# Optimization experiments

Measured on AMD Instinct MI355X. Metric: run time of the kernel, lower is better.

## Reference

```python
import jax, jax.numpy as jnp
import numpy as np

NUM_HEADS = 8
HEAD_DIM = 64


def setup_inputs() -> dict:
    key = jax.random.key(0)
    k1, k2, k3 = jax.random.split(key, 3)
    B, T, S, D = 2, 32, 1024, 512
    inner = NUM_HEADS * HEAD_DIM  # 512
    x = jax.random.normal(k1, (B, T, S, D), dtype=jnp.float32)
    W_qkv = jax.random.normal(k2, (D, 3 * inner), dtype=jnp.float32) * (D ** -0.5)
    W_out = jax.random.normal(k3, (inner, D), dtype=jnp.float32) * (inner ** -0.5)
    return {"x": x, "W_qkv": W_qkv, "W_out": W_out}


def reference(x, W_qkv, W_out):
    # x: (B, T, S, D); causal attention over T at each spatial position S.
    B, T, S, D = x.shape
    H, hd = NUM_HEADS, HEAD_DIM
    scale = hd ** -0.5
    qkv = jnp.einsum('btsd,de->btse', x, W_qkv)  # (B,T,S,3*H*hd)
    qkv = qkv.reshape(B, T, S, 3, H, hd)
    q, k, v = qkv[..., 0, :, :], qkv[..., 1, :, :], qkv[..., 2, :, :]  # (B,T,S,H,hd)
    # attention logits per (batch, spatial, head): (B,S,H,Tq,Tk)
    attn = jnp.einsum('bqshd,bkshd->bshqk', q, k) * scale
    causal_mask = jnp.triu(jnp.ones((T, T), dtype=bool), 1)  # True above diagonal
    attn = jnp.where(causal_mask, -jnp.inf, attn)
    attn = jax.nn.softmax(attn, axis=-1)
    out = jnp.einsum('bshqk,bkshd->bqshd', attn, v)  # (B,T,S,H,hd)
    out = out.reshape(B, T, S, H * hd)
    return jnp.einsum('btse,ed->btsd', out, W_out)  # (B,T,S,D)
```

## Files before the change

kernel.cpp:

```cpp
#include <hip/hip_runtime.h>
#include <cstdint>
#include <cstddef>

#define KDIM 512

typedef __attribute__((ext_vector_type(8))) __bf16 bf16x8;
typedef __attribute__((ext_vector_type(8))) unsigned short ushort8;
typedef __attribute__((ext_vector_type(4))) float f32x4;
typedef unsigned short u16;

__device__ __forceinline__ float bf2f(u16 u) {
  union { unsigned u32; float f; } x; x.u32 = ((unsigned)u) << 16; return x.f;
}
__device__ __forceinline__ u16 f2bf(float f) {
  union { float f; unsigned u; } x; x.f = f;
  unsigned u = x.u;
  unsigned r = (u + 0x7fffu + ((u >> 16) & 1u)) >> 16;
  return (u16)r;
}

__global__ __launch_bounds__(256) void cast_x_kernel(const float* __restrict__ in,
                                                     u16* __restrict__ out, int n4) {
  int i = blockIdx.x * 256 + threadIdx.x;
  if (i >= n4) return;
  float4 v = ((const float4*)in)[i];
  ushort4 o;
  o.x = f2bf(v.x); o.y = f2bf(v.y); o.z = f2bf(v.z); o.w = f2bf(v.w);
  ((ushort4*)out)[i] = o;
}

__global__ __launch_bounds__(256) void transpose_cast_kernel(const float* __restrict__ in,
                                                             u16* __restrict__ out,
                                                             int R, int C) {
  int o = blockIdx.x * 256 + threadIdx.x;
  if (o >= R * C) return;
  int r = o % R;
  int c = o / R;
  out[o] = f2bf(in[(size_t)r * C + c]);
}

__device__ __forceinline__ void gload_lds16(const void* g, void* l) {
  __builtin_amdgcn_global_load_lds((__attribute__((address_space(1))) unsigned int*)g,
                                   (__attribute__((address_space(3))) unsigned int*)l,
                                   16, 0, 0);
}

template <typename OutT>
__global__ __launch_bounds__(512, 2) void gemm256_kernel(const u16* __restrict__ A,
                                                         const u16* __restrict__ Bt,
                                                         OutT* __restrict__ C,
                                                         int N, int NXT) {
  __shared__ __attribute__((aligned(16))) u16 As[2][256 * 64];
  __shared__ __attribute__((aligned(16))) u16 Bs[2][256 * 64];
  const int tid = threadIdx.x;
  const int wid = tid >> 6, l = tid & 63;
  const int wm = wid >> 2, wn = wid & 3;
  const int g = l >> 4, i = l & 15;

  const int nwg = gridDim.x;
  const int cpx = nwg >> 3;
  const int bid = blockIdx.x;
  const int swz = (bid & 7) * cpx + (bid >> 3);
  const int mt = swz / NXT, nt = swz % NXT;
  const size_t m0 = (size_t)mt * 256, n0 = (size_t)nt * 256;

  const int srow = l >> 3;
  const int sblk = (l & 7) ^ srow;

  f32x4 acc[8][4] = {};

  auto STAGE = [&](int buf, int t) {
    const int k0 = t << 6;
#pragma unroll
    for (int j = 0; j < 4; ++j) {
      int c = wid * 4 + j;
      gload_lds16(A + (m0 + c * 8 + srow) * KDIM + k0 + sblk * 8, &As[buf][c * 512]);
    }
#pragma unroll
    for (int j = 0; j < 4; ++j) {
      int c = wid * 4 + j;
      gload_lds16(Bt + (n0 + c * 8 + srow) * KDIM + k0 + sblk * 8, &Bs[buf][c * 512]);
    }
  };

  auto COMPUTE = [&](int buf) {
#pragma unroll
    for (int ks = 0; ks < 2; ++ks) {
      const int sw = ((ks * 4 + g) ^ (i & 7)) * 8;
      bf16x8 af[8], bv[4];
#pragma unroll
      for (int m = 0; m < 8; ++m)
        af[m] = *(const bf16x8*)&As[buf][(wm * 128 + m * 16 + i) * 64 + sw];
#pragma unroll
      for (int n = 0; n < 4; ++n)
        bv[n] = *(const bf16x8*)&Bs[buf][(wn * 64 + n * 16 + i) * 64 + sw];
      __builtin_amdgcn_s_setprio(1);
#pragma unroll
      for (int m = 0; m < 8; ++m)
#pragma unroll
        for (int n = 0; n < 4; ++n)
          acc[m][n] = __builtin_amdgcn_mfma_f32_16x16x32_bf16(af[m], bv[n], acc[m][n], 0, 0, 0);
      __builtin_amdgcn_s_setprio(0);
    }
  };

  STAGE(0, 0);
  STAGE(1, 1);
  for (int t = 0; t < 7; ++t) {
    asm volatile("s_waitcnt vmcnt(8)" ::: "memory");
    __builtin_amdgcn_s_barrier();
    __builtin_amdgcn_sched_barrier(0);
    COMPUTE(t & 1);
    __builtin_amdgcn_sched_barrier(0);
    __builtin_amdgcn_s_barrier();
    __builtin_amdgcn_sched_barrier(0);
    if (t < 6) STAGE(t & 1, t + 2);
  }
  asm volatile("s_waitcnt vmcnt(0)" ::: "memory");
  __builtin_amdgcn_s_barrier();
  __builtin_amdgcn_sched_barrier(0);
  COMPUTE(1);

#pragma unroll
  for (int m = 0; m < 8; ++m) {
    size_t rowb = m0 + wm * 128 + m * 16 + g * 4;
#pragma unroll
    for (int n = 0; n < 4; ++n) {
      size_t colg = n0 + wn * 64 + n * 16 + i;
#pragma unroll
      for (int r = 0; r < 4; ++r) {
        size_t idx = (rowb + r) * (size_t)N + colg;
        if constexpr (sizeof(OutT) == 2) C[idx] = (OutT)f2bf(acc[m][n][r]);
        else C[idx] = acc[m][n][r];
      }
    }
  }
}

__global__ __launch_bounds__(256, 4) void attn_mfma_kernel(const u16* __restrict__ qkv,
                                                           u16* __restrict__ out) {
  const int bs = blockIdx.x >> 1;
  const int hg = blockIdx.x & 1;
  const int b = bs >> 10, s = bs & 1023;
  __shared__ __attribute__((aligned(16))) u16 Ks[4][2048];
  __shared__ __attribute__((aligned(16))) u16 Vt[4][2048];
  __shared__ __attribute__((aligned(16))) u16 Ps[4][1024];

  const int tid = threadIdx.x;
  const int wv = tid >> 6;
  const int h = hg * 4 + wv;
  const int l = tid & 63;
  const int g = l >> 4, i = l & 15;

  const size_t tstride = (size_t)1024 * 1536;
  const size_t base = ((size_t)(b * 32) * 1024 + s) * 1536;

  {
    const int krow = l >> 3;
    const int dbs = (l & 7) ^ krow;
#pragma unroll
    for (int j = 0; j < 4; ++j) {
      int k = j * 8 + krow;
      gload_lds16(qkv + base + (size_t)k * tstride + 512 + h * 64 + dbs * 8, &Ks[wv][j * 512]);
    }
  }

  const int vk = l & 31;
  ushort8 vv[4];
#pragma unroll
  for (int j = 0; j < 4; ++j) {
    int c = (l >> 5) + 2 * j;
    vv[j] = *(const ushort8*)(qkv + base + (size_t)vk * tstride + 1024 + h * 64 + c * 8);
  }

  bf16x8 bq[2][2];
#pragma unroll
  for (int n = 0; n < 2; ++n)
#pragma unroll
    for (int ks = 0; ks < 2; ++ks)
      bq[n][ks] = *(const bf16x8*)(qkv + base + (size_t)(n * 16 + i) * tstride + h * 64 + ks * 32 + g * 8);

#pragma unroll
  for (int j = 0; j < 4; ++j) {
    int c = (l >> 5) + 2 * j;
#pragma unroll
    for (int u = 0; u < 8; ++u) {
      int d = c * 8 + u;
      int pos = (vk >> 3) ^ (d & 3);
      Vt[wv][d * 32 + pos * 8 + (vk & 7)] = vv[j][u];
    }
  }

  asm volatile("s_waitcnt vmcnt(0)" ::: "memory");

  f32x4 sc[2][2] = {};
#pragma unroll
  for (int m = 0; m < 2; ++m)
#pragma unroll
    for (int ks = 0; ks < 2; ++ks) {
      int k = m * 16 + i;
      int pos = (ks * 4 + g) ^ (k & 7);
      bf16x8 ak = *(const bf16x8*)&Ks[wv][k * 64 + pos * 8];
      sc[m][0] = __builtin_amdgcn_mfma_f32_16x16x32_bf16(ak, bq[0][ks], sc[m][0], 0, 0, 0);
      sc[m][1] = __builtin_amdgcn_mfma_f32_16x16x32_bf16(ak, bq[1][ks], sc[m][1], 0, 0, 0);
    }

  float p[2][2][4];
#pragma unroll
  for (int n = 0; n < 2; ++n) {
    int q = n * 16 + i;
    float m0 = -1e30f;
#pragma unroll
    for (int m = 0; m < 2; ++m)
#pragma unroll
      for (int r = 0; r < 4; ++r) {
        int k = m * 16 + g * 4 + r;
        float v = (k <= q) ? sc[m][n][r] * 0.125f : -1e30f;
        p[m][n][r] = v;
        m0 = fmaxf(m0, v);
      }
    m0 = fmaxf(m0, __shfl_xor(m0, 16));
    m0 = fmaxf(m0, __shfl_xor(m0, 32));
    float s0 = 0.f;
#pragma unroll
    for (int m = 0; m < 2; ++m)
#pragma unroll
      for (int r = 0; r < 4; ++r) {
        float e = __expf(p[m][n][r] - m0);
        p[m][n][r] = e;
        s0 += e;
      }
    s0 += __shfl_xor(s0, 16);
    s0 += __shfl_xor(s0, 32);
    float inv = 1.f / s0;
#pragma unroll
    for (int m = 0; m < 2; ++m)
#pragma unroll
      for (int r = 0; r < 4; ++r) p[m][n][r] *= inv;
  }

#pragma unroll
  for (int m = 0; m < 2; ++m)
#pragma unroll
    for (int n = 0; n < 2; ++n) {
      int q = n * 16 + i;
      int kb = m * 2 + (g >> 1);
      int pos = kb ^ (q & 3);
      uint2 wo;
      wo.x = (unsigned)f2bf(p[m][n][0]) | ((unsigned)f2bf(p[m][n][1]) << 16);
      wo.y = (unsigned)f2bf(p[m][n][2]) | ((unsigned)f2bf(p[m][n][3]) << 16);
      *(uint2*)&Ps[wv][q * 32 + pos * 8 + (g & 1) * 4] = wo;
    }

  asm volatile("s_waitcnt lgkmcnt(0)" ::: "memory");

  bf16x8 bv[4];
#pragma unroll
  for (int np = 0; np < 4; ++np) {
    int d = np * 16 + i;
    int pos = g ^ (d & 3);
    bv[np] = *(const bf16x8*)&Vt[wv][d * 32 + pos * 8];
  }
  f32x4 o[2][4] = {};
#pragma unroll
  for (int mp = 0; mp < 2; ++mp) {
    int q = mp * 16 + i;
    int pos = g ^ (q & 3);
    bf16x8 ap = *(const bf16x8*)&Ps[wv][q * 32 + pos * 8];
#pragma unroll
    for (int np = 0; np < 4; ++np)
      o[mp][np] = __builtin_amdgcn_mfma_f32_16x16x32_bf16(ap, bv[np], o[mp][np], 0, 0, 0);
  }

#pragma unroll
  for (int mp = 0; mp < 2; ++mp)
#pragma unroll
    for (int r = 0; r < 4; ++r) {
      int q = mp * 16 + g * 4 + r;
      u16* dst = out + ((size_t)((b * 32 + q) * 1024 + s)) * 512 + h * 64;
#pragma unroll
      for (int np = 0; np < 4; ++np)
        dst[np * 16 + i] = f2bf(o[mp][np][r]);
    }
}

extern "C" void kernel_launch(void* const* d_in, const int* in_sizes, int n_in,
                              void* d_out, int out_size, void* d_ws, size_t ws_size,
                              hipStream_t stream) {
  const float* x = (const float*)d_in[0];
  const float* Wqkv = (const float*)d_in[1];
  const float* Wout = (const float*)d_in[2];
  float* outp = (float*)d_out;

  char* ws = (char*)d_ws;
  u16* x_bf = (u16*)(ws);
  u16* qkv_bf = (u16*)(ws + (size_t)67108864);
  u16* wqkv_t = (u16*)(ws + (size_t)268435456);
  u16* wout_t = (u16*)(ws + (size_t)270008320);
  u16* attn_o = x_bf;

  cast_x_kernel<<<32768, 256, 0, stream>>>(x, x_bf, 8388608);
  transpose_cast_kernel<<<3072, 256, 0, stream>>>(Wqkv, wqkv_t, 512, 1536);
  transpose_cast_kernel<<<1024, 256, 0, stream>>>(Wout, wout_t, 512, 512);

  gemm256_kernel<u16><<<1536, 512, 0, stream>>>(x_bf, wqkv_t, qkv_bf, 1536, 6);

  attn_mfma_kernel<<<4096, 256, 0, stream>>>(qkv_bf, attn_o);

  gemm256_kernel<float><<<512, 512, 0, stream>>>(attn_o, wout_t, outp, 512, 2);
}
```

Measured before the change: 302.1 us.

## Switch GEMM to 4-slot K=32 pipeline with single barrier per step

Restructures the bf16 GEMM main loop from double-buffered K=64 tiles to a four-slot ring of K=32 tiles, keeping three loads in flight. The next tile is issued before compute, so only one barrier per iteration is needed. The LDS layout and XOR swizzle change to match 32-wide rows. This halves the MFMA work per barrier and adds more iterations, and the vmcnt accounting must be exactly right for the ring to be safe.

```diff
diff --git a/kernel.cpp b/kernel.cpp
--- a/kernel.cpp
+++ b/kernel.cpp
@@ -50,8 +50,8 @@
                                                          const u16* __restrict__ Bt,
                                                          OutT* __restrict__ C,
                                                          int N, int NXT) {
-  __shared__ __attribute__((aligned(16))) u16 As[2][256 * 64];
-  __shared__ __attribute__((aligned(16))) u16 Bs[2][256 * 64];
+  __shared__ __attribute__((aligned(16))) u16 As[4][8192];
+  __shared__ __attribute__((aligned(16))) u16 Bs[4][8192];
   const int tid = threadIdx.x;
   const int wid = tid >> 6, l = tid & 63;
   const int wm = wid >> 2, wn = wid & 3;
@@ -64,62 +64,61 @@
   const int mt = swz / NXT, nt = swz % NXT;
   const size_t m0 = (size_t)mt * 256, n0 = (size_t)nt * 256;
 
-  const int srow = l >> 3;
-  const int sblk = (l & 7) ^ srow;
+  const int srow = tid >> 2;
+  const int sbp = tid & 3;
+  const int sbs = sbp ^ ((srow >> 1) & 3);
 
   f32x4 acc[8][4] = {};
 
-  auto STAGE = [&](int buf, int t) {
-    const int k0 = t << 6;
-#pragma unroll
-    for (int j = 0; j < 4; ++j) {
-      int c = wid * 4 + j;
-      gload_lds16(A + (m0 + c * 8 + srow) * KDIM + k0 + sblk * 8, &As[buf][c * 512]);
-    }
-#pragma unroll
-    for (int j = 0; j < 4; ++j) {
-      int c = wid * 4 + j;
-      gload_lds16(Bt + (n0 + c * 8 + srow) * KDIM + k0 + sblk * 8, &Bs[buf][c * 512]);
-    }
+  auto STAGE = [&](int t, int slot) {
+    const int k0 = t << 5;
+    gload_lds16(A + (m0 + srow) * KDIM + k0 + sbs * 8, &As[slot][tid * 8]);
+    gload_lds16(A + (m0 + 128 + srow) * KDIM + k0 + sbs * 8, &As[slot][(tid + 512) * 8]);
+    gload_lds16(Bt + (n0 + srow) * KDIM + k0 + sbs * 8, &Bs[slot][tid * 8]);
+    gload_lds16(Bt + (n0 + 128 + srow) * KDIM + k0 + sbs * 8, &Bs[slot][(tid + 512) * 8]);
   };
 
-  auto COMPUTE = [&](int buf) {
-#pragma unroll
-    for (int ks = 0; ks < 2; ++ks) {
-      const int sw = ((ks * 4 + g) ^ (i & 7)) * 8;
-      bf16x8 af[8], bv[4];
-#pragma unroll
-      for (int m = 0; m < 8; ++m)
-        af[m] = *(const bf16x8*)&As[buf][(wm * 128 + m * 16 + i) * 64 + sw];
+  auto COMPUTE = [&](int slot) {
+    bf16x8 af[8], bv[4];
+#pragma unroll
+    for (int m = 0; m < 8; ++m) {
+      int row = wm * 128 + m * 16 + i;
+      af[m] = *(const bf16x8*)&As[slot][row * 32 + ((g ^ ((row >> 1) & 3)) << 3)];
+    }
+#pragma unroll
+    for (int n = 0; n < 4; ++n) {
+      int row = wn * 64 + n * 16 + i;
+      bv[n] = *(const bf16x8*)&Bs[slot][row * 32 + ((g ^ ((row >> 1) & 3)) << 3)];
+    }
+    __builtin_amdgcn_s_setprio(1);
+#pragma unroll
+    for (int m = 0; m < 8; ++m)
 #pragma unroll
       for (int n = 0; n < 4; ++n)
-        bv[n] = *(const bf16x8*)&Bs[buf][(wn * 64 + n * 16 + i) * 64 + sw];
-      __builtin_amdgcn_s_setprio(1);
-#pragma unroll
-      for (int m = 0; m < 8; ++m)
-#pragma unroll
-        for (int n = 0; n < 4; ++n)
-          acc[m][n] = __builtin_amdgcn_mfma_f32_16x16x32_bf16(af[m], bv[n], acc[m][n], 0, 0, 0);
-      __builtin_amdgcn_s_setprio(0);
-    }
+        acc[m][n] = __builtin_amdgcn_mfma_f32_16x16x32_bf16(af[m], bv[n], acc[m][n], 0, 0, 0);
+    __builtin_amdgcn_s_setprio(0);
   };
 
   STAGE(0, 0);
   STAGE(1, 1);
-  for (int t = 0; t < 7; ++t) {
+  STAGE(2, 2);
+  for (int t = 0; t < 14; ++t) {
     asm volatile("s_waitcnt vmcnt(8)" ::: "memory");
     __builtin_amdgcn_s_barrier();
     __builtin_amdgcn_sched_barrier(0);
-    COMPUTE(t & 1);
+    if (t < 13) STAGE(t + 3, (t + 3) & 3);
+    COMPUTE(t & 3);
     __builtin_amdgcn_sched_barrier(0);
-    __builtin_amdgcn_s_barrier();
-    __builtin_amdgcn_sched_barrier(0);
-    if (t < 6) STAGE(t & 1, t + 2);
-  }
+  }
+  asm volatile("s_waitcnt vmcnt(4)" ::: "memory");
+  __builtin_amdgcn_s_barrier();
+  __builtin_amdgcn_sched_barrier(0);
+  COMPUTE(2);
+  __builtin_amdgcn_sched_barrier(0);
   asm volatile("s_waitcnt vmcnt(0)" ::: "memory");
   __builtin_amdgcn_s_barrier();
   __builtin_amdgcn_sched_barrier(0);
-  COMPUTE(1);
+  COMPUTE(3);
 
 #pragma unroll
   for (int m = 0; m < 8; ++m) {
```

Result: slower. 308.8 us (+2.2%).

## Restructure GEMM main loop into quarter phases interleaving loads with MFMA

Applied to the files above, without the earlier changes.

The 256x256 bf16 GEMM loop is rewritten so each K-step runs in four phases. Each phase issues one half-tile global-to-LDS load for the next buffer, prefetches the next A fragments from LDS, and runs a slice of MFMAs, with barriers between phases. The goal is to spread memory traffic across the compute instead of staging whole tiles between barriers. In exchange it adds many more barriers per iteration, waits on vmcnt(0) at the end of each step, and prefetches only one tile ahead instead of two.

```diff
diff --git a/kernel.cpp b/kernel.cpp
--- a/kernel.cpp
+++ b/kernel.cpp
@@ -46,12 +46,12 @@
 }
 
 template <typename OutT>
-__global__ __launch_bounds__(512, 2) void gemm256_kernel(const u16* __restrict__ A,
-                                                         const u16* __restrict__ Bt,
-                                                         OutT* __restrict__ C,
-                                                         int N, int NXT) {
-  __shared__ __attribute__((aligned(16))) u16 As[2][256 * 64];
-  __shared__ __attribute__((aligned(16))) u16 Bs[2][256 * 64];
+__global__ __launch_bounds__(512, 2) void gemm8p_kernel(const u16* __restrict__ A,
+                                                        const u16* __restrict__ Bt,
+                                                        OutT* __restrict__ C,
+                                                        int N, int NXT) {
+  __shared__ __attribute__((aligned(16))) u16 As[2][16384];
+  __shared__ __attribute__((aligned(16))) u16 Bs[2][16384];
   const int tid = threadIdx.x;
   const int wid = tid >> 6, l = tid & 63;
   const int wm = wid >> 2, wn = wid & 3;
@@ -64,62 +64,85 @@
   const int mt = swz / NXT, nt = swz % NXT;
   const size_t m0 = (size_t)mt * 256, n0 = (size_t)nt * 256;
 
-  const int srow = l >> 3;
-  const int sblk = (l & 7) ^ srow;
-
   f32x4 acc[8][4] = {};
 
-  auto STAGE = [&](int buf, int t) {
-    const int k0 = t << 6;
-#pragma unroll
-    for (int j = 0; j < 4; ++j) {
-      int c = wid * 4 + j;
-      gload_lds16(A + (m0 + c * 8 + srow) * KDIM + k0 + sblk * 8, &As[buf][c * 512]);
-    }
-#pragma unroll
-    for (int j = 0; j < 4; ++j) {
-      int c = wid * 4 + j;
-      gload_lds16(Bt + (n0 + c * 8 + srow) * KDIM + k0 + sblk * 8, &Bs[buf][c * 512]);
+  auto STAGE_HALF = [&](const u16* G, u16* L, size_t gr0, int h, int k0) {
+#pragma unroll
+    for (int j = 0; j < 2; ++j) {
+      int rowl = (tid >> 3) + (j << 6);
+      int row = (h << 7) + rowl;
+      int bbs = (tid & 7) ^ (row & 7);
+      gload_lds16(G + (gr0 + row) * KDIM + k0 + bbs * 8,
+                  L + (h << 13) + (((j << 9) + tid) << 3));
     }
   };
 
-  auto COMPUTE = [&](int buf) {
-#pragma unroll
-    for (int ks = 0; ks < 2; ++ks) {
-      const int sw = ((ks * 4 + g) ^ (i & 7)) * 8;
-      bf16x8 af[8], bv[4];
-#pragma unroll
-      for (int m = 0; m < 8; ++m)
-        af[m] = *(const bf16x8*)&As[buf][(wm * 128 + m * 16 + i) * 64 + sw];
-#pragma unroll
-      for (int n = 0; n < 4; ++n)
-        bv[n] = *(const bf16x8*)&Bs[buf][(wn * 64 + n * 16 + i) * 64 + sw];
-      __builtin_amdgcn_s_setprio(1);
-#pragma unroll
-      for (int m = 0; m < 8; ++m)
-#pragma unroll
-        for (int n = 0; n < 4; ++n)
-          acc[m][n] = __builtin_amdgcn_mfma_f32_16x16x32_bf16(af[m], bv[n], acc[m][n], 0, 0, 0);
-      __builtin_amdgcn_s_setprio(0);
-    }
-  };
-
-  STAGE(0, 0);
-  STAGE(1, 1);
-  for (int t = 0; t < 7; ++t) {
-    asm volatile("s_waitcnt vmcnt(8)" ::: "memory");
-    __builtin_amdgcn_s_barrier();
-    __builtin_amdgcn_sched_barrier(0);
-    COMPUTE(t & 1);
-    __builtin_amdgcn_sched_barrier(0);
-    __builtin_amdgcn_s_barrier();
-    __builtin_amdgcn_sched_barrier(0);
-    if (t < 6) STAGE(t & 1, t + 2);
-  }
+  STAGE_HALF(A, &As[0][0], m0, 0, 0);
+  STAGE_HALF(A, &As[0][0], m0, 1, 0);
+  STAGE_HALF(Bt, &Bs[0][0], n0, 0, 0);
+  STAGE_HALF(Bt, &Bs[0][0], n0, 1, 0);
   asm volatile("s_waitcnt vmcnt(0)" ::: "memory");
   __builtin_amdgcn_s_barrier();
   __builtin_amdgcn_sched_barrier(0);
-  COMPUTE(1);
+
+  for (int t = 0; t < 8; ++t) {
+    const int buf = t & 1;
+    const int k0n = (t + 1) << 6;
+    const u16* Ab = &As[buf][0];
+    const u16* Bb = &Bs[buf][0];
+
+    bf16x8 bv[2][4];
+#pragma unroll
+    for (int ks = 0; ks < 2; ++ks)
+#pragma unroll
+      for (int n = 0; n < 4; ++n) {
+        int row = wn * 64 + n * 16 + i;
+        bv[ks][n] = *(const bf16x8*)&Bb[row * 64 + (((ks * 4 + g) ^ (row & 7)) << 3)];
+      }
+    bf16x8 afr[2][2][2];
+#pragma unroll
+    for (int ks = 0; ks < 2; ++ks)
+#pragma unroll
+      for (int mm = 0; mm < 2; ++mm) {
+        int row = wm * 128 + mm * 16 + i;
+        afr[0][ks][mm] = *(const bf16x8*)&Ab[row * 64 + (((ks * 4 + g) ^ (row & 7)) << 3)];
+      }
+
+#pragma unroll
+    for (int q = 0; q < 4; ++q) {
+      if (q < 3) {
+#pragma unroll
+        for (int ks = 0; ks < 2; ++ks)
+#pragma unroll
+          for (int mm = 0; mm < 2; ++mm) {
+            int row = wm * 128 + (q + 1) * 32 + mm * 16 + i;
+            afr[(q + 1) & 1][ks][mm] =
+                *(const bf16x8*)&Ab[row * 64 + (((ks * 4 + g) ^ (row & 7)) << 3)];
+          }
+      }
+      if (t < 7) {
+        if (q == 0) STAGE_HALF(A, &As[buf ^ 1][0], m0, 0, k0n);
+        else if (q == 1) STAGE_HALF(A, &As[buf ^ 1][0], m0, 1, k0n);
+        else if (q == 2) STAGE_HALF(Bt, &Bs[buf ^ 1][0], n0, 0, k0n);
+        else STAGE_HALF(Bt, &Bs[buf ^ 1][0], n0, 1, k0n);
+      }
+      __builtin_amdgcn_s_barrier();
+      __builtin_amdgcn_s_setprio(1);
+#pragma unroll
+      for (int ks = 0; ks < 2; ++ks)
+#pragma unroll
+        for (int mm = 0; mm < 2; ++mm)
+#pragma unroll
+          for (int n = 0; n < 4; ++n)
+            acc[q * 2 + mm][n] = __builtin_amdgcn_mfma_f32_16x16x32_bf16(
+                afr[q & 1][ks][mm], bv[ks][n], acc[q * 2 + mm][n], 0, 0, 0);
+      __builtin_amdgcn_s_setprio(0);
+      if (q < 3) __builtin_amdgcn_s_barrier();
+    }
+    if (t < 7) asm volatile("s_waitcnt vmcnt(0)" ::: "memory");
+    __builtin_amdgcn_s_barrier();
+    __builtin_amdgcn_sched_barrier(0);
+  }
 
 #pragma unroll
   for (int m = 0; m < 8; ++m) {
@@ -303,9 +326,9 @@
   transpose_cast_kernel<<<3072, 256, 0, stream>>>(Wqkv, wqkv_t, 512, 1536);
   transpose_cast_kernel<<<1024, 256, 0, stream>>>(Wout, wout_t, 512, 512);
 
-  gemm256_kernel<u16><<<1536, 512, 0, stream>>>(x_bf, wqkv_t, qkv_bf, 1536, 6);
+  gemm8p_kernel<u16><<<1536, 512, 0, stream>>>(x_bf, wqkv_t, qkv_bf, 1536, 6);
 
   attn_mfma_kernel<<<4096, 256, 0, stream>>>(qkv_bf, attn_o);
 
-  gemm256_kernel<float><<<512, 512, 0, stream>>>(attn_o, wout_t, outp, 512, 2);
-}
+  gemm8p_kernel<float><<<512, 512, 0, stream>>>(attn_o, wout_t, outp, 512, 2);
+}
```

Measured after the change: 308.8 us. 1.02x slower.
